# Kernel tuning notes

Hardware: AMD Instinct MI355X
Metric: run time of the kernel (lower is better)

The kernel has to match this reference:

```python
import jax, jax.numpy as jnp
import numpy as np

N_NODES = 50000
N_EDGES = 800000
IN_DIM = 256
HID = 64
HEADS = 4
NUM_GRAPHS = 8
NEG_SLOPE = 0.2  # PyG GATConv default


def setup_inputs() -> dict:
    key = jax.random.key(0)
    ks = jax.random.split(key, 14)
    x = jax.random.normal(ks[0], (N_NODES, IN_DIM), jnp.float32)
    edge_index = jax.random.randint(ks[1], (2, N_EDGES), 0, N_NODES, jnp.int32)
    batch = jnp.sort(jax.random.randint(ks[2], (N_NODES,), 0, NUM_GRAPHS, jnp.int32))
    s1 = 1.0 / np.sqrt(IN_DIM)
    s2 = 1.0 / np.sqrt(HID * HEADS)
    W1 = jax.random.normal(ks[3], (IN_DIM, HEADS * HID), jnp.float32) * s1
    a_src1 = jax.random.normal(ks[4], (HEADS, HID), jnp.float32) * (1.0 / np.sqrt(HID))
    a_dst1 = jax.random.normal(ks[5], (HEADS, HID), jnp.float32) * (1.0 / np.sqrt(HID))
    b1 = jnp.zeros((HEADS * HID,), jnp.float32)
    W2 = jax.random.normal(ks[6], (HEADS * HID, HID), jnp.float32) * s2
    a_src2 = jax.random.normal(ks[7], (1, HID), jnp.float32) * (1.0 / np.sqrt(HID))
    a_dst2 = jax.random.normal(ks[8], (1, HID), jnp.float32) * (1.0 / np.sqrt(HID))
    b2 = jnp.zeros((HID,), jnp.float32)
    fcW = jax.random.normal(ks[9], (HID, 2), jnp.float32) * (1.0 / np.sqrt(HID))
    fcb = jnp.zeros((2,), jnp.float32)
    return {"x": x, "edge_index": edge_index, "batch": batch,
            "W1": W1, "a_src1": a_src1, "a_dst1": a_dst1, "b1": b1,
            "W2": W2, "a_src2": a_src2, "a_dst2": a_dst2, "b2": b2,
            "fcW": fcW, "fcb": fcb}


def _gat_layer(x, src, dst, W, a_src, a_dst, b, heads, out_dim, concat):
    """PyG-style GATConv: gather -> edge attention -> segment softmax -> scatter-add."""
    N = x.shape[0]
    xw = (x @ W).reshape(N, heads, out_dim)          # [N,H,C]
    al = jnp.einsum('nhc,hc->nh', xw, a_src)         # alpha_src per node
    ar = jnp.einsum('nhc,hc->nh', xw, a_dst)         # alpha_dst per node
    e = jax.nn.leaky_relu(al[src] + ar[dst], NEG_SLOPE)  # [E,H]
    m = jax.ops.segment_max(e, dst, num_segments=N)      # stable softmax per dst
    w = jnp.exp(e - m[dst])
    denom = jax.ops.segment_sum(w, dst, num_segments=N)
    alpha = w / denom[dst]                               # [E,H]
    out = jax.ops.segment_sum(alpha[:, :, None] * xw[src], dst, num_segments=N)  # [N,H,C]
    out = out.reshape(N, heads * out_dim) if concat else out.mean(axis=1)
    return out + b


def reference(x, edge_index, batch, W1, a_src1, a_dst1, b1, W2, a_src2, a_dst2, b2, fcW, fcb):
    N = x.shape[0]
    loops = jnp.arange(N, dtype=edge_index.dtype)  # PyG add_self_loops=True default
    src = jnp.concatenate([edge_index[0], loops])
    dst = jnp.concatenate([edge_index[1], loops])
    h = jax.nn.elu(_gat_layer(x, src, dst, W1, a_src1, a_dst1, b1, HEADS, HID, True))
    h = jax.nn.elu(_gat_layer(h, src, dst, W2, a_src2, a_dst2, b2, 1, HID, True))
    ssum = jax.ops.segment_sum(h, batch, num_segments=NUM_GRAPHS)
    cnt = jax.ops.segment_sum(jnp.ones((N, 1), h.dtype), batch, num_segments=NUM_GRAPHS)
    pooled = ssum / jnp.maximum(cnt, 1.0)  # global_mean_pool
    logits = pooled @ fcW + fcb
    return (h, logits)
```

## Files before the change

kernel.cpp:

```cpp
#include <hip/hip_runtime.h>

#define NEG_SLOPE 0.2f
#define NG 8
#define CH 64

typedef unsigned short ushort_t;

__device__ __forceinline__ float lrelu(float x) { return x > 0.f ? x : NEG_SLOPE * x; }
__device__ __forceinline__ float eluf(float x) { return x > 0.f ? x : expm1f(x); }
__device__ __forceinline__ float wave_sum(float v) {
    #pragma unroll
    for (int o = 32; o; o >>= 1) v += __shfl_xor(v, o);
    return v;
}
__device__ __forceinline__ ushort_t f2bf(float f) {
    unsigned u = __float_as_uint(f);
    unsigned r = (u + 0x7FFFu + ((u >> 16) & 1u)) >> 16;
    return (ushort_t)r;
}
__device__ __forceinline__ float bf2f(ushort_t s) {
    return __uint_as_float(((unsigned)s) << 16);
}

__global__ __launch_bounds__(256) void k_hist(const int* __restrict__ ei,
                                              int* __restrict__ deg, int E) {
    int e = blockIdx.x * 256 + threadIdx.x;
    if (e < E) atomicAdd(&deg[ei[E + e]], 1);
}

__global__ __launch_bounds__(256) void k_scanA(const int* __restrict__ deg,
                                               int* __restrict__ bsum, int N) {
    __shared__ int wsums[4];
    int b = blockIdx.x, t = threadIdx.x;
    int base = b * 1024 + t * 4;
    int s = 0;
    #pragma unroll
    for (int k = 0; k < 4; k++) { int i = base + k; if (i < N) s += deg[i]; }
    #pragma unroll
    for (int o = 32; o; o >>= 1) s += __shfl_xor(s, o);
    if ((t & 63) == 0) wsums[t >> 6] = s;
    __syncthreads();
    if (t == 0) bsum[b] = wsums[0] + wsums[1] + wsums[2] + wsums[3];
}

__global__ __launch_bounds__(64) void k_scanB(const int* __restrict__ bsum,
                                              int* __restrict__ boff,
                                              int* __restrict__ rpN, int SB) {
    int lane = threadIdx.x;
    int own = (lane < SB) ? bsum[lane] : 0;
    int v = own;
    #pragma unroll
    for (int o = 1; o < 64; o <<= 1) { int y = __shfl_up(v, o); if (lane >= o) v += y; }
    if (lane < SB) boff[lane] = v - own;
    if (lane == 63) *rpN = v;
}

__global__ __launch_bounds__(256) void k_scanC(const int* __restrict__ deg,
                                               const int* __restrict__ boff,
                                               int* __restrict__ rp,
                                               int* __restrict__ cur, int N) {
    __shared__ int wtot[4];
    int b = blockIdx.x, t = threadIdx.x;
    int wid = t >> 6, lane = t & 63;
    int base = b * 1024 + t * 4;
    int d[4];
    #pragma unroll
    for (int k = 0; k < 4; k++) d[k] = (base + k < N) ? deg[base + k] : 0;
    int tsum = d[0] + d[1] + d[2] + d[3];
    int v = tsum;
    #pragma unroll
    for (int o = 1; o < 64; o <<= 1) { int y = __shfl_up(v, o); if (lane >= o) v += y; }
    if (lane == 63) wtot[wid] = v;
    __syncthreads();
    int wbase = 0;
    for (int k = 0; k < wid; k++) wbase += wtot[k];
    int run = boff[b] + wbase + v - tsum;
    #pragma unroll
    for (int k = 0; k < 4; k++) {
        if (base + k < N) { rp[base + k] = run; cur[base + k] = run; }
        run += d[k];
    }
}

__global__ __launch_bounds__(256) void k_fill(const int* __restrict__ ei,
                                              int* __restrict__ cur,
                                              int* __restrict__ csr, int E) {
    int e = blockIdx.x * 256 + threadIdx.x;
    if (e >= E) return;
    int s = ei[e], d = ei[E + e];
    int pos = atomicAdd(&cur[d], 1);
    csr[pos] = s;
}

__global__ __launch_bounds__(256, 5) void k_gemm1(const float* __restrict__ x,
                                               const float* __restrict__ W1,
                                               const float* __restrict__ a_s,
                                               const float* __restrict__ a_d,
                                               ushort_t* __restrict__ xw1b,
                                               float* __restrict__ al4,
                                               float* __restrict__ ar4, int N) {
    __shared__ float As[32][256];
    int r0 = blockIdx.x * 32;
    int lane = threadIdx.x & 63, rq = threadIdx.x >> 6;
    int c4 = lane << 2;
    for (int i = threadIdx.x; i < 2048; i += 256) {
        int r = i >> 6, k4 = (i & 63) << 2;
        float4 v = (r0 + r < N) ? *(const float4*)(x + (size_t)(r0 + r) * 256 + k4)
                                : make_float4(0.f, 0.f, 0.f, 0.f);
        As[r][k4] = v.x; As[r][k4 + 1] = v.y; As[r][k4 + 2] = v.z; As[r][k4 + 3] = v.w;
    }
    __syncthreads();
    float4 acc[8];
    #pragma unroll
    for (int t = 0; t < 8; t++) acc[t] = make_float4(0.f, 0.f, 0.f, 0.f);
    float4 w0 = *(const float4*)(W1 + (size_t)0 * 256 + c4);
    float4 w1 = *(const float4*)(W1 + (size_t)1 * 256 + c4);
    float4 w2 = *(const float4*)(W1 + (size_t)2 * 256 + c4);
    float4 w3 = *(const float4*)(W1 + (size_t)3 * 256 + c4);
    for (int k4 = 0; k4 < 256; k4 += 4) {
        int kn = (k4 + 4 < 256) ? (k4 + 4) : 0;
        const float* Wn = W1 + (size_t)kn * 256 + c4;
        float4 n0 = *(const float4*)(Wn + 0);
        float4 n1 = *(const float4*)(Wn + 256);
        float4 n2 = *(const float4*)(Wn + 512);
        float4 n3 = *(const float4*)(Wn + 768);
        #pragma unroll
        for (int t = 0; t < 8; t++) {
            float4 a = *(const float4*)(&As[rq + 4 * t][k4]);
            acc[t].x += a.x * w0.x + a.y * w1.x + a.z * w2.x + a.w * w3.x;
            acc[t].y += a.x * w0.y + a.y * w1.y + a.z * w2.y + a.w * w3.y;
            acc[t].z += a.x * w0.z + a.y * w1.z + a.z * w2.z + a.w * w3.z;
            acc[t].w += a.x * w0.w + a.y * w1.w + a.z * w2.w + a.w * w3.w;
        }
        w0 = n0; w1 = n1; w2 = n2; w3 = n3;
    }
    int h = lane >> 4, kk = c4 & 63;
    float4 s4 = *(const float4*)(a_s + h * 64 + kk);
    float4 d4 = *(const float4*)(a_d + h * 64 + kk);
    #pragma unroll
    for (int t = 0; t < 8; t++) {
        float sl = acc[t].x * s4.x + acc[t].y * s4.y + acc[t].z * s4.z + acc[t].w * s4.w;
        float sr = acc[t].x * d4.x + acc[t].y * d4.y + acc[t].z * d4.z + acc[t].w * d4.w;
        #pragma unroll
        for (int o = 1; o < 16; o <<= 1) { sl += __shfl_xor(sl, o); sr += __shfl_xor(sr, o); }
        int r = r0 + rq + 4 * t;
        if ((lane & 15) == 0 && r < N) {
            al4[(size_t)r * 4 + h] = sl;
            ar4[(size_t)r * 4 + h] = sr;
        }
    }
    __syncthreads();
    ushort_t* Ls = (ushort_t*)As;
    #pragma unroll
    for (int t = 0; t < 8; t++) {
        int rl = rq + 4 * t;
        Ls[rl * 256 + (kk + 0) * 4 + h] = f2bf(acc[t].x);
        Ls[rl * 256 + (kk + 1) * 4 + h] = f2bf(acc[t].y);
        Ls[rl * 256 + (kk + 2) * 4 + h] = f2bf(acc[t].z);
        Ls[rl * 256 + (kk + 3) * 4 + h] = f2bf(acc[t].w);
    }
    __syncthreads();
    #pragma unroll
    for (int p = 0; p < 4; p++) {
        int flat = p * 2048 + threadIdx.x * 8;
        int rl = flat >> 8, col = flat & 255;
        int r = r0 + rl;
        if (r < N)
            *(uint4*)(xw1b + (size_t)r * 256 + col) = *(const uint4*)(Ls + flat);
    }
}

__device__ __forceinline__ float4 wexp4(float4 a, float4 arn) {
    float4 w;
    w.x = __expf(lrelu(a.x + arn.x));
    w.y = __expf(lrelu(a.y + arn.y));
    w.z = __expf(lrelu(a.z + arn.z));
    w.w = __expf(lrelu(a.w + arn.w));
    return w;
}

__device__ __forceinline__ void gather1(int n, int lane,
                                        const int* __restrict__ rp,
                                        const int* __restrict__ csr,
                                        const float* __restrict__ al4,
                                        const float* __restrict__ ar4,
                                        const ushort_t* __restrict__ xw1b,
                                        const float* __restrict__ b1,
                                        float4* __restrict__ wb,
                                        int* __restrict__ sb,
                                        float* __restrict__ hrow) {
    int e0 = rp[n], e1 = rp[n + 1];
    float4 arn = *(const float4*)(ar4 + (size_t)n * 4);
    float4 aln = *(const float4*)(al4 + (size_t)n * 4);
    float4 wsf = wexp4(aln, arn);
    ushort4 sv = *(const ushort4*)(xw1b + (size_t)n * 256 + lane * 4);
    float a0 = wsf.x * bf2f(sv.x);
    float a1 = wsf.y * bf2f(sv.y);
    float a2 = wsf.z * bf2f(sv.z);
    float a3 = wsf.w * bf2f(sv.w);
    float px = 0.f, py = 0.f, pz = 0.f, pw = 0.f;
    for (int cs = e0; cs < e1; cs += CH) {
        int cnt = min(CH, e1 - cs);
        if (lane < cnt) {
            int s = csr[cs + lane];
            float4 A = *(const float4*)(al4 + (size_t)s * 4);
            float4 w = wexp4(A, arn);
            sb[lane] = s;
            wb[lane] = w;
            px += w.x; py += w.y; pz += w.z; pw += w.w;
        }
        asm volatile("s_waitcnt lgkmcnt(0)" ::: "memory");
        int jj = 0;
        for (; jj + 4 <= cnt; jj += 4) {
            int s0 = sb[jj],     s1 = sb[jj + 1];
            int s2 = sb[jj + 2], s3 = sb[jj + 3];
            float4 w0 = wb[jj],     w1 = wb[jj + 1];
            float4 w2 = wb[jj + 2], w3 = wb[jj + 3];
            ushort4 v0 = *(const ushort4*)(xw1b + (size_t)s0 * 256 + lane * 4);
            ushort4 v1 = *(const ushort4*)(xw1b + (size_t)s1 * 256 + lane * 4);
            ushort4 v2 = *(const ushort4*)(xw1b + (size_t)s2 * 256 + lane * 4);
            ushort4 v3 = *(const ushort4*)(xw1b + (size_t)s3 * 256 + lane * 4);
            a0 += w0.x * bf2f(v0.x) + w1.x * bf2f(v1.x) + w2.x * bf2f(v2.x) + w3.x * bf2f(v3.x);
            a1 += w0.y * bf2f(v0.y) + w1.y * bf2f(v1.y) + w2.y * bf2f(v2.y) + w3.y * bf2f(v3.y);
            a2 += w0.z * bf2f(v0.z) + w1.z * bf2f(v1.z) + w2.z * bf2f(v2.z) + w3.z * bf2f(v3.z);
            a3 += w0.w * bf2f(v0.w) + w1.w * bf2f(v1.w) + w2.w * bf2f(v2.w) + w3.w * bf2f(v3.w);
        }
        for (; jj < cnt; jj++) {
            int s = sb[jj];
            float4 w = wb[jj];
            ushort4 v = *(const ushort4*)(xw1b + (size_t)s * 256 + lane * 4);
            a0 += w.x * bf2f(v.x);
            a1 += w.y * bf2f(v.y);
            a2 += w.z * bf2f(v.z);
            a3 += w.w * bf2f(v.w);
        }
    }
    float wx = wave_sum(px) + wsf.x;
    float wy = wave_sum(py) + wsf.y;
    float wz = wave_sum(pz) + wsf.z;
    float ww = wave_sum(pw) + wsf.w;
    hrow[lane]       = eluf(a0 / wx + b1[lane]);
    hrow[64 + lane]  = eluf(a1 / wy + b1[64 + lane]);
    hrow[128 + lane] = eluf(a2 / wz + b1[128 + lane]);
    hrow[192 + lane] = eluf(a3 / ww + b1[192 + lane]);
}

__global__ __launch_bounds__(256, 8) void k_agg4(const int* __restrict__ rp,
                                                 const int* __restrict__ csr,
                                                 const float* __restrict__ al4,
                                                 const float* __restrict__ ar4,
                                                 const ushort_t* __restrict__ xw1b,
                                                 const float* __restrict__ b1,
                                                 const float* __restrict__ W2,
                                                 const float* __restrict__ as2,
                                                 const float* __restrict__ ad2,
                                                 ushort_t* __restrict__ xw2b,
                                                 float* __restrict__ al2,
                                                 float* __restrict__ ar2, int N) {
    __shared__ float hs[4][512];
    __shared__ float4 wbuf[4][CH];
    __shared__ int sbuf[4][CH];
    int wIdx = threadIdx.x >> 6;
    int w = (blockIdx.x * 256 + threadIdx.x) >> 6;
    int lane = threadIdx.x & 63;
    int nA = 2 * w, nB = 2 * w + 1;
    if (nA >= N) return;
    bool hasB = (nB < N);
    gather1(nA, lane, rp, csr, al4, ar4, xw1b, b1, wbuf[wIdx], sbuf[wIdx],
            &hs[wIdx][0]);
    if (hasB)
        gather1(nB, lane, rp, csr, al4, ar4, xw1b, b1, wbuf[wIdx], sbuf[wIdx],
                &hs[wIdx][256]);
    asm volatile("s_waitcnt lgkmcnt(0)" ::: "memory");
    {
        float accA = 0.f, accB = 0.f;
        const float* w2l = W2 + lane;
        #pragma unroll 2
        for (int k4 = 0; k4 < 64; k4++) {
            float u0 = w2l[(size_t)(k4 * 4 + 0) * 64];
            float u1 = w2l[(size_t)(k4 * 4 + 1) * 64];
            float u2 = w2l[(size_t)(k4 * 4 + 2) * 64];
            float u3 = w2l[(size_t)(k4 * 4 + 3) * 64];
            float4 hA = *(const float4*)(&hs[wIdx][k4 * 4]);
            accA += hA.x * u0 + hA.y * u1 + hA.z * u2 + hA.w * u3;
            if (hasB) {
                float4 hB = *(const float4*)(&hs[wIdx][256 + k4 * 4]);
                accB += hB.x * u0 + hB.y * u1 + hB.z * u2 + hB.w * u3;
            }
        }
        xw2b[(size_t)nA * 64 + lane] = f2bf(accA);
        float slA = wave_sum(accA * as2[lane]);
        float srA = wave_sum(accA * ad2[lane]);
        if (lane == 0) { al2[nA] = slA; ar2[nA] = srA; }
        if (hasB) {
            xw2b[(size_t)nB * 64 + lane] = f2bf(accB);
            float slB = wave_sum(accB * as2[lane]);
            float srB = wave_sum(accB * ad2[lane]);
            if (lane == 0) { al2[nB] = slB; ar2[nB] = srB; }
        }
    }
}

__global__ __launch_bounds__(256, 8) void k_agg2(const int* __restrict__ rp,
                                                 const int* __restrict__ csr,
                                                 const float* __restrict__ al2,
                                                 const float* __restrict__ ar2,
                                                 const ushort_t* __restrict__ xw2b,
                                                 const float* __restrict__ b2,
                                                 float* __restrict__ hout, int N) {
    __shared__ float wbuf[4][CH];
    __shared__ int sbuf[4][CH];
    int wIdx = threadIdx.x >> 6;
    int n = (blockIdx.x * 256 + threadIdx.x) >> 6;
    int lane = threadIdx.x & 63;
    if (n >= N) return;
    int e0 = rp[n], e1 = rp[n + 1];
    float arn = ar2[n];
    float wself = __expf(lrelu(al2[n] + arn));
    float acc = wself * bf2f(xw2b[(size_t)n * 64 + lane]);
    float p = 0.f;
    for (int cs = e0; cs < e1; cs += CH) {
        int cnt = min(CH, e1 - cs);
        if (lane < cnt) {
            int s = csr[cs + lane];
            float w = __expf(lrelu(al2[s] + arn));
            sbuf[wIdx][lane] = s;
            wbuf[wIdx][lane] = w;
            p += w;
        }
        asm volatile("s_waitcnt lgkmcnt(0)" ::: "memory");
        int jj = 0;
        for (; jj + 8 <= cnt; jj += 8) {
            int s0 = sbuf[wIdx][jj],     s1 = sbuf[wIdx][jj + 1];
            int s2 = sbuf[wIdx][jj + 2], s3 = sbuf[wIdx][jj + 3];
            int s4 = sbuf[wIdx][jj + 4], s5 = sbuf[wIdx][jj + 5];
            int s6 = sbuf[wIdx][jj + 6], s7 = sbuf[wIdx][jj + 7];
            float w0 = wbuf[wIdx][jj],     w1 = wbuf[wIdx][jj + 1];
            float w2 = wbuf[wIdx][jj + 2], w3 = wbuf[wIdx][jj + 3];
            float w4 = wbuf[wIdx][jj + 4], w5 = wbuf[wIdx][jj + 5];
            float w6 = wbuf[wIdx][jj + 6], w7 = wbuf[wIdx][jj + 7];
            float v0 = bf2f(xw2b[(size_t)s0 * 64 + lane]);
            float v1 = bf2f(xw2b[(size_t)s1 * 64 + lane]);
            float v2 = bf2f(xw2b[(size_t)s2 * 64 + lane]);
            float v3 = bf2f(xw2b[(size_t)s3 * 64 + lane]);
            float v4 = bf2f(xw2b[(size_t)s4 * 64 + lane]);
            float v5 = bf2f(xw2b[(size_t)s5 * 64 + lane]);
            float v6 = bf2f(xw2b[(size_t)s6 * 64 + lane]);
            float v7 = bf2f(xw2b[(size_t)s7 * 64 + lane]);
            acc += w0 * v0 + w1 * v1 + w2 * v2 + w3 * v3;
            acc += w4 * v4 + w5 * v5 + w6 * v6 + w7 * v7;
        }
        for (; jj + 4 <= cnt; jj += 4) {
            int s0 = sbuf[wIdx][jj],     s1 = sbuf[wIdx][jj + 1];
            int s2 = sbuf[wIdx][jj + 2], s3 = sbuf[wIdx][jj + 3];
            float w0 = wbuf[wIdx][jj],     w1 = wbuf[wIdx][jj + 1];
            float w2 = wbuf[wIdx][jj + 2], w3 = wbuf[wIdx][jj + 3];
            float v0 = bf2f(xw2b[(size_t)s0 * 64 + lane]);
            float v1 = bf2f(xw2b[(size_t)s1 * 64 + lane]);
            float v2 = bf2f(xw2b[(size_t)s2 * 64 + lane]);
            float v3 = bf2f(xw2b[(size_t)s3 * 64 + lane]);
            acc += w0 * v0 + w1 * v1 + w2 * v2 + w3 * v3;
        }
        for (; jj < cnt; jj++) {
            int s = sbuf[wIdx][jj];
            acc += wbuf[wIdx][jj] * bf2f(xw2b[(size_t)s * 64 + lane]);
        }
    }
    float wsum = wave_sum(p) + wself;
    hout[(size_t)n * 64 + lane] = eluf(acc / wsum + b2[lane]);
}

__global__ __launch_bounds__(256) void k_pool(const float* __restrict__ h2,
                                              const int* __restrict__ batch,
                                              float* __restrict__ pooled,
                                              float* __restrict__ cnt, int N) {
    int wave = (blockIdx.x * 256 + threadIdx.x) >> 6;
    int lane = threadIdx.x & 63;
    int n0 = wave * 32;
    if (n0 >= N) return;
    int n1 = min(n0 + 32, N);
    float acc = 0.f; int cl = 0;
    int curg = batch[n0];
    for (int n = n0; n < n1; n++) {
        int g = batch[n];
        if (g != curg) {
            atomicAdd(&pooled[curg * 64 + lane], acc);
            if (lane == 0) atomicAdd(&cnt[curg], (float)cl);
            acc = 0.f; cl = 0; curg = g;
        }
        acc += h2[(size_t)n * 64 + lane];
        cl++;
    }
    atomicAdd(&pooled[curg * 64 + lane], acc);
    if (lane == 0) atomicAdd(&cnt[curg], (float)cl);
}

__global__ __launch_bounds__(64) void k_logits(const float* __restrict__ pooled,
                                               const float* __restrict__ cnt,
                                               const float* __restrict__ fcW,
                                               const float* __restrict__ fcb,
                                               float* __restrict__ out) {
    int t = threadIdx.x;
    if (t >= NG * 2) return;
    int g = t >> 1, o = t & 1;
    float invc = 1.f / fmaxf(cnt[g], 1.f);
    float s = 0.f;
    for (int c = 0; c < 64; c++)
        s += pooled[g * 64 + c] * invc * fcW[c * 2 + o];
    s += fcb[o];
    out[g * 2 + o] = s;
}

extern "C" void kernel_launch(void* const* d_in, const int* in_sizes, int n_in,
                              void* d_out, int out_size, void* d_ws, size_t ws_size,
                              hipStream_t stream) {
    const float* x     = (const float*)d_in[0];
    const int*   ei    = (const int*)d_in[1];
    const int*   batch = (const int*)d_in[2];
    const float* W1    = (const float*)d_in[3];
    const float* as1   = (const float*)d_in[4];
    const float* ad1   = (const float*)d_in[5];
    const float* b1    = (const float*)d_in[6];
    const float* W2    = (const float*)d_in[7];
    const float* as2   = (const float*)d_in[8];
    const float* ad2   = (const float*)d_in[9];
    const float* b2v   = (const float*)d_in[10];
    const float* fcW   = (const float*)d_in[11];
    const float* fcb   = (const float*)d_in[12];
    float* out = (float*)d_out;

    const int N = in_sizes[2];
    const int E = in_sizes[1] / 2;
    const size_t nv  = (size_t)N * 64;
    const size_t nv4 = (size_t)N * 256;
    const int SB = (N + 1023) / 1024;

    ushort_t* xw1b = (ushort_t*)d_ws;
    ushort_t* xw2b   = xw1b + nv4;
    float*    al4    = (float*)(xw2b + nv);
    float*    ar4    = al4 + (size_t)N * 4;
    float*    al2    = ar4 + (size_t)N * 4;
    float*    ar2    = al2 + N;
    float*    pooled = ar2 + N;
    float*    cnt    = pooled + NG * 64;
    int*      deg    = (int*)(cnt + 8);
    int*      rp     = deg + N;
    int*      cur    = rp + N + 1;
    int*      csr    = cur + N;
    int*      bsum   = csr + E;
    int*      boff   = bsum + 64;

    const int gE  = (E + 255) / 256;
    const int gB4 = (N + 7) / 8;
    const int gB2 = (N + 3) / 4;
    const int gG1 = (N + 31) / 32;
    const int pw  = (N + 31) / 32;
    const int gP  = (pw * 64 + 255) / 256;

    hipMemsetAsync(deg, 0, (size_t)N * sizeof(int), stream);
    k_hist<<<gE, 256, 0, stream>>>(ei, deg, E);
    k_scanA<<<SB, 256, 0, stream>>>(deg, bsum, N);
    k_scanB<<<1, 64, 0, stream>>>(bsum, boff, rp + N, SB);
    k_scanC<<<SB, 256, 0, stream>>>(deg, boff, rp, cur, N);
    k_fill<<<gE, 256, 0, stream>>>(ei, cur, csr, E);

    k_gemm1<<<gG1, 256, 0, stream>>>(x, W1, as1, ad1, xw1b, al4, ar4, N);
    k_agg4<<<gB4, 256, 0, stream>>>(rp, csr, al4, ar4, xw1b, b1, W2, as2, ad2,
                                    xw2b, al2, ar2, N);

    k_agg2<<<gB2, 256, 0, stream>>>(rp, csr, al2, ar2, xw2b, b2v, out, N);

    hipMemsetAsync(pooled, 0, (NG * 64 + NG) * sizeof(float), stream);
    k_pool<<<gP, 256, 0, stream>>>(out, batch, pooled, cnt, N);
    k_logits<<<1, 64, 0, stream>>>(pooled, cnt, fcW, fcb, out + nv);
}
```

Baseline: 517.6 us.

## Use split-bf16 MFMA for layer-1 projection GEMM

Replaces the FP32 FMA GEMM in k_gemm1 with bf16 MFMA 16x16x32 instructions. Near-FP32 accuracy is kept by splitting x and W1 into high and low bf16 parts and issuing three MFMAs per tile. A new small kernel transposes and splits W1 each call. The accumulators then go through shared memory so the attention dot products and the bf16 packing work as before. This cuts the compute cost of the GEMM, at the price of an extra kernel launch, more shared memory and slightly different rounding.

```diff
diff --git a/kernel.cpp b/kernel.cpp
--- a/kernel.cpp
+++ b/kernel.cpp
@@ -5,6 +5,8 @@
 #define CH 64
 
 typedef unsigned short ushort_t;
+typedef __attribute__((ext_vector_type(8))) short short8v;
+typedef __attribute__((ext_vector_type(4))) float f32x4;
 
 __device__ __forceinline__ float lrelu(float x) { return x > 0.f ? x : NEG_SLOPE * x; }
 __device__ __forceinline__ float eluf(float x) { return x > 0.f ? x : expm1f(x); }
@@ -92,77 +94,112 @@
     csr[pos] = s;
 }
 
-__global__ __launch_bounds__(256, 5) void k_gemm1(const float* __restrict__ x,
-                                               const float* __restrict__ W1,
+__global__ __launch_bounds__(256) void k_w1t(const float* __restrict__ W1,
+                                             ushort_t* __restrict__ w1th,
+                                             ushort_t* __restrict__ w1tl) {
+    int c = blockIdx.x, k = threadIdx.x;
+    float w = W1[(size_t)k * 256 + c];
+    ushort_t hi = f2bf(w);
+    float lo = w - bf2f(hi);
+    w1th[c * 256 + k] = hi;
+    w1tl[c * 256 + k] = f2bf(lo);
+}
+
+__global__ __launch_bounds__(256, 4) void k_gemm1(const float* __restrict__ x,
+                                               const ushort_t* __restrict__ w1th,
+                                               const ushort_t* __restrict__ w1tl,
                                                const float* __restrict__ a_s,
                                                const float* __restrict__ a_d,
                                                ushort_t* __restrict__ xw1b,
                                                float* __restrict__ al4,
                                                float* __restrict__ ar4, int N) {
-    __shared__ float As[32][256];
+    __shared__ __align__(16) unsigned char smem[33792];
+    ushort_t* xh = (ushort_t*)smem;
+    ushort_t* xl = (ushort_t*)(smem + 16896);
     int r0 = blockIdx.x * 32;
-    int lane = threadIdx.x & 63, rq = threadIdx.x >> 6;
-    int c4 = lane << 2;
-    for (int i = threadIdx.x; i < 2048; i += 256) {
+    int tid = threadIdx.x;
+    int lane = tid & 63, wv = tid >> 6;
+    for (int i = tid; i < 2048; i += 256) {
         int r = i >> 6, k4 = (i & 63) << 2;
         float4 v = (r0 + r < N) ? *(const float4*)(x + (size_t)(r0 + r) * 256 + k4)
                                 : make_float4(0.f, 0.f, 0.f, 0.f);
-        As[r][k4] = v.x; As[r][k4 + 1] = v.y; As[r][k4 + 2] = v.z; As[r][k4 + 3] = v.w;
-    }
-    __syncthreads();
-    float4 acc[8];
-    #pragma unroll
-    for (int t = 0; t < 8; t++) acc[t] = make_float4(0.f, 0.f, 0.f, 0.f);
-    float4 w0 = *(const float4*)(W1 + (size_t)0 * 256 + c4);
-    float4 w1 = *(const float4*)(W1 + (size_t)1 * 256 + c4);
-    float4 w2 = *(const float4*)(W1 + (size_t)2 * 256 + c4);
-    float4 w3 = *(const float4*)(W1 + (size_t)3 * 256 + c4);
-    for (int k4 = 0; k4 < 256; k4 += 4) {
-        int kn = (k4 + 4 < 256) ? (k4 + 4) : 0;
-        const float* Wn = W1 + (size_t)kn * 256 + c4;
-        float4 n0 = *(const float4*)(Wn + 0);
-        float4 n1 = *(const float4*)(Wn + 256);
-        float4 n2 = *(const float4*)(Wn + 512);
-        float4 n3 = *(const float4*)(Wn + 768);
+        ushort4 h4, l4;
+        h4.x = f2bf(v.x); l4.x = f2bf(v.x - bf2f(h4.x));
+        h4.y = f2bf(v.y); l4.y = f2bf(v.y - bf2f(h4.y));
+        h4.z = f2bf(v.z); l4.z = f2bf(v.z - bf2f(h4.z));
+        h4.w = f2bf(v.w); l4.w = f2bf(v.w - bf2f(h4.w));
+        *(ushort4*)(&xh[r * 264 + k4]) = h4;
+        *(ushort4*)(&xl[r * 264 + k4]) = l4;
+    }
+    __syncthreads();
+    int wr = wv & 1, wc = wv >> 1;
+    int jl = lane & 15, q = lane >> 4;
+    f32x4 acc[8];
+    #pragma unroll
+    for (int t = 0; t < 8; t++) acc[t] = (f32x4){0.f, 0.f, 0.f, 0.f};
+    const ushort_t* xhp = &xh[(16 * wr + jl) * 264];
+    const ushort_t* xlp = &xl[(16 * wr + jl) * 264];
+    #pragma unroll 1
+    for (int ks = 0; ks < 8; ks++) {
+        int ko = 32 * ks + 8 * q;
+        short8v ah = *(const short8v*)(xhp + ko);
+        short8v alo = *(const short8v*)(xlp + ko);
         #pragma unroll
         for (int t = 0; t < 8; t++) {
-            float4 a = *(const float4*)(&As[rq + 4 * t][k4]);
-            acc[t].x += a.x * w0.x + a.y * w1.x + a.z * w2.x + a.w * w3.x;
-            acc[t].y += a.x * w0.y + a.y * w1.y + a.z * w2.y + a.w * w3.y;
-            acc[t].z += a.x * w0.z + a.y * w1.z + a.z * w2.z + a.w * w3.z;
-            acc[t].w += a.x * w0.w + a.y * w1.w + a.z * w2.w + a.w * w3.w;
-        }
-        w0 = n0; w1 = n1; w2 = n2; w3 = n3;
-    }
+            int c0 = 128 * wc + 16 * t;
+            short8v bh = *(const short8v*)(w1th + (size_t)(c0 + jl) * 256 + ko);
+            short8v bl = *(const short8v*)(w1tl + (size_t)(c0 + jl) * 256 + ko);
+            acc[t] = __builtin_amdgcn_mfma_f32_16x16x32_bf16(ah, bh, acc[t], 0, 0, 0);
+            acc[t] = __builtin_amdgcn_mfma_f32_16x16x32_bf16(ah, bl, acc[t], 0, 0, 0);
+            acc[t] = __builtin_amdgcn_mfma_f32_16x16x32_bf16(alo, bh, acc[t], 0, 0, 0);
+        }
+    }
+    __syncthreads();
+    float* outb = (float*)smem;
+    #pragma unroll
+    for (int t = 0; t < 8; t++) {
+        int c = 128 * wc + 16 * t + jl;
+        int rb = 16 * wr + 4 * q;
+        outb[(rb + 0) * 256 + c] = acc[t].x;
+        outb[(rb + 1) * 256 + c] = acc[t].y;
+        outb[(rb + 2) * 256 + c] = acc[t].z;
+        outb[(rb + 3) * 256 + c] = acc[t].w;
+    }
+    __syncthreads();
+    int c4 = lane << 2;
     int h = lane >> 4, kk = c4 & 63;
     float4 s4 = *(const float4*)(a_s + h * 64 + kk);
     float4 d4 = *(const float4*)(a_d + h * 64 + kk);
-    #pragma unroll
-    for (int t = 0; t < 8; t++) {
-        float sl = acc[t].x * s4.x + acc[t].y * s4.y + acc[t].z * s4.z + acc[t].w * s4.w;
-        float sr = acc[t].x * d4.x + acc[t].y * d4.y + acc[t].z * d4.z + acc[t].w * d4.w;
+    float4 hv[8];
+    #pragma unroll
+    for (int t2 = 0; t2 < 8; t2++)
+        hv[t2] = *(const float4*)(&outb[(wv + 4 * t2) * 256 + c4]);
+    #pragma unroll
+    for (int t2 = 0; t2 < 8; t2++) {
+        float sl = hv[t2].x * s4.x + hv[t2].y * s4.y + hv[t2].z * s4.z + hv[t2].w * s4.w;
+        float sr = hv[t2].x * d4.x + hv[t2].y * d4.y + hv[t2].z * d4.z + hv[t2].w * d4.w;
         #pragma unroll
         for (int o = 1; o < 16; o <<= 1) { sl += __shfl_xor(sl, o); sr += __shfl_xor(sr, o); }
-        int r = r0 + rq + 4 * t;
+        int r = r0 + wv + 4 * t2;
         if ((lane & 15) == 0 && r < N) {
             al4[(size_t)r * 4 + h] = sl;
             ar4[(size_t)r * 4 + h] = sr;
         }
     }
     __syncthreads();
-    ushort_t* Ls = (ushort_t*)As;
-    #pragma unroll
-    for (int t = 0; t < 8; t++) {
-        int rl = rq + 4 * t;
-        Ls[rl * 256 + (kk + 0) * 4 + h] = f2bf(acc[t].x);
-        Ls[rl * 256 + (kk + 1) * 4 + h] = f2bf(acc[t].y);
-        Ls[rl * 256 + (kk + 2) * 4 + h] = f2bf(acc[t].z);
-        Ls[rl * 256 + (kk + 3) * 4 + h] = f2bf(acc[t].w);
+    ushort_t* Ls = (ushort_t*)smem;
+    #pragma unroll
+    for (int t2 = 0; t2 < 8; t2++) {
+        int rl = wv + 4 * t2;
+        Ls[rl * 256 + (kk + 0) * 4 + h] = f2bf(hv[t2].x);
+        Ls[rl * 256 + (kk + 1) * 4 + h] = f2bf(hv[t2].y);
+        Ls[rl * 256 + (kk + 2) * 4 + h] = f2bf(hv[t2].z);
+        Ls[rl * 256 + (kk + 3) * 4 + h] = f2bf(hv[t2].w);
     }
     __syncthreads();
     #pragma unroll
     for (int p = 0; p < 4; p++) {
-        int flat = p * 2048 + threadIdx.x * 8;
+        int flat = p * 2048 + tid * 8;
         int rl = flat >> 8, col = flat & 255;
         int r = r0 + rl;
         if (r < N)
@@ -449,6 +486,8 @@
     int*      csr    = cur + N;
     int*      bsum   = csr + E;
     int*      boff   = bsum + 64;
+    ushort_t* w1th = (ushort_t*)(((uintptr_t)(boff + 64) + 255) & ~(uintptr_t)255);
+    ushort_t* w1tl = w1th + 65536;
 
     const int gE  = (E + 255) / 256;
     const int gB4 = (N + 7) / 8;
@@ -463,8 +502,9 @@
     k_scanB<<<1, 64, 0, stream>>>(bsum, boff, rp + N, SB);
     k_scanC<<<SB, 256, 0, stream>>>(deg, boff, rp, cur, N);
     k_fill<<<gE, 256, 0, stream>>>(ei, cur, csr, E);
-
-    k_gemm1<<<gG1, 256, 0, stream>>>(x, W1, as1, ad1, xw1b, al4, ar4, N);
+    k_w1t<<<256, 256, 0, stream>>>(W1, w1th, w1tl);
+
+    k_gemm1<<<gG1, 256, 0, stream>>>(x, w1th, w1tl, as1, ad1, xw1b, al4, ar4, N);
     k_agg4<<<gB4, 256, 0, stream>>>(rp, csr, al4, ar4, xw1b, b1, W2, as2, ad2,
                                     xw2b, al2, ar2, N);
 
```

After: 511.1 us. Within noise of the previous version (-1.3%).
